# Kernel tuning notes

Hardware: AMD Instinct MI355X
Metric: run time of the kernel (lower is better)

The kernel has to match this reference:

```python
import jax, jax.numpy as jnp
import numpy as np

B, T, D = 16384, 7, 1024
H = D // 2          # LSTM hidden = 512
E = 64              # num_experts
TOPK = 8
NFLOW = 4


def setup_inputs() -> dict:
    key = jax.random.key(0)
    ks = jax.random.split(key, 16)
    s = 0.05
    return {
        'x': jax.random.normal(ks[0], (B, D), jnp.float32),
        'context': jax.random.normal(ks[1], (B, T, D), jnp.float32),
        # LSTM (PyTorch layout: [4H, in], gate order i,f,g,o)
        'W_ih': jax.random.normal(ks[2], (4 * H, D), jnp.float32) * s,
        'W_hh': jax.random.normal(ks[3], (4 * H, H), jnp.float32) * s,
        'b_ih': jnp.zeros((4 * H,), jnp.float32),
        'b_hh': jnp.zeros((4 * H,), jnp.float32),
        # flow_detector: Linear(D,H) -> ReLU -> Linear(H,4) -> softmax
        'fw1': jax.random.normal(ks[4], (H, D), jnp.float32) * s,
        'fb1': jnp.zeros((H,), jnp.float32),
        'fw2': jax.random.normal(ks[5], (NFLOW, H), jnp.float32) * s,
        'fb2': jnp.zeros((NFLOW,), jnp.float32),
        # main_gate: Linear(D+H+4, D) -> ReLU -> Linear(D, E)
        'gw1': jax.random.normal(ks[6], (D, D + H + NFLOW), jnp.float32) * s,
        'gb1': jnp.zeros((D,), jnp.float32),
        'gw2': jax.random.normal(ks[7], (E, D), jnp.float32) * s,
        'gb2': jnp.zeros((E,), jnp.float32),
        'expert_spec': jax.random.normal(ks[8], (E, NFLOW), jnp.float32) * 0.1,
    }


def _lstm_last_hidden(context, W_ih, W_hh, b_ih, b_hh):
    """Single-layer LSTM over [B,T,D]; returns last hidden state [B,H]."""
    b = b_ih + b_hh
    xs = jnp.einsum('btd,gd->tbg', context, W_ih) + b  # [T,B,4H], precompute input proj

    def step(carry, x_t):
        h, c = carry
        gates = x_t + h @ W_hh.T
        i, f, g, o = jnp.split(gates, 4, axis=-1)
        c = jax.nn.sigmoid(f) * c + jax.nn.sigmoid(i) * jnp.tanh(g)
        h = jax.nn.sigmoid(o) * jnp.tanh(c)
        return (h, c), None

    h0 = jnp.zeros((context.shape[0], H), context.dtype)
    (h, _), _ = jax.lax.scan(step, (h0, h0), xs)
    return h


def reference(x, context, W_ih, W_hh, b_ih, b_hh, fw1, fb1, fw2, fb2,
              gw1, gb1, gw2, gb2, expert_spec):
    context_feature = _lstm_last_hidden(context, W_ih, W_hh, b_ih, b_hh)  # [B,H]

    # flow_detector
    flow_state = jax.nn.softmax(
        jax.nn.relu(x @ fw1.T + fb1) @ fw2.T + fb2, axis=-1)  # [B,4]

    combined = jnp.concatenate([x, context_feature, flow_state], axis=-1)  # [B, D+H+4]
    gate_logits = jax.nn.relu(combined @ gw1.T + gb1) @ gw2.T + gb2  # [B,E]

    specialization = flow_state @ expert_spec.T  # [B,E]
    adjusted_logits = gate_logits + 0.1 * specialization
    gate_probs = jax.nn.softmax(adjusted_logits, axis=-1)

    top_k_probs, top_k_indices = jax.lax.top_k(gate_probs, TOPK)
    top_k_probs = top_k_probs / (top_k_probs.sum(-1, keepdims=True) + 1e-8)

    expert_usage = gate_probs.mean(0)  # [E]
    uniform = jnp.full_like(expert_usage, 1.0 / E)
    # F.kl_div(log_input, target, reduction='batchmean'): sum(t*(log t - log_input))/E
    load_balancing_loss = jnp.sum(
        uniform * (jnp.log(uniform) - jnp.log(expert_usage))) / E

    return (top_k_probs, top_k_indices, load_balancing_loss,
            flow_state, expert_usage, adjusted_logits)
```

## Files before the change

### kernel.cpp

```cpp
#include <hip/hip_runtime.h>
#include <cmath>

#define NB    16384
#define NT    7
#define ND    1024
#define NH    512
#define NE    64

#define OFF_WCAT   0ll
#define OFF_BLSTM  3145728ll
#define OFF_GW1P   3147776ll
#define OFF_FW1P   4737024ll
#define OFF_GW2T   5261312ll
#define OFF_H0     5326848ll
#define OFF_H1     13715456ll
#define OFF_C      22104064ll
#define OFF_HID    30492672ll
#define OFF_FLOW   47269888ll
#define OFF_UACC   47335424ll
#define WS_FLOATS  47335488ll

#define OUT_TOPKP  0ll
#define OUT_IDX    131072ll
#define OUT_LOSS   262144ll
#define OUT_FLOW   262145ll
#define OUT_USAGE  327681ll
#define OUT_ADJ    327745ll

__device__ __forceinline__ float sigm(float x) { return 1.0f / (1.0f + expf(-x)); }

__global__ void pack_lstm_k(const float* __restrict__ Wih, const float* __restrict__ Whh,
                            const float* __restrict__ bih, const float* __restrict__ bhh,
                            float* __restrict__ wcat, float* __restrict__ bl) {
  int idx = blockIdx.x * 256 + threadIdx.x;
  if (idx < 1536 * 2048) {
    int k = idx >> 11, n = idx & 2047;
    int u = n >> 2, g = n & 3;
    int r = g * 512 + u;
    wcat[idx] = (k < 1024) ? Wih[(size_t)r * 1024 + k] : Whh[(size_t)r * 512 + (k - 1024)];
  }
  if (idx < 2048) {
    int u = idx >> 2, g = idx & 3;
    int r = g * 512 + u;
    bl[idx] = bih[r] + bhh[r];
  }
}

__global__ void pack_gw1_k(const float* __restrict__ gw1, float* __restrict__ gw1p) {
  int idx = blockIdx.x * 256 + threadIdx.x;
  if (idx < 1552 * 1024) {
    int k = idx >> 10, n = idx & 1023;
    gw1p[idx] = (k < 1540) ? gw1[(size_t)n * 1540 + k] : 0.0f;
  }
}

__global__ void pack_fw1_k(const float* __restrict__ fw1, float* __restrict__ fw1p) {
  int idx = blockIdx.x * 256 + threadIdx.x;
  if (idx < 1024 * 512) {
    int k = idx >> 9, n = idx & 511;
    fw1p[idx] = fw1[(size_t)n * 1024 + k];
  }
}

__global__ void pack_gw2t_k(const float* __restrict__ gw2, float* __restrict__ gw2t) {
  int idx = blockIdx.x * 256 + threadIdx.x;
  if (idx < 1024 * 64) {
    int k = idx >> 6, e = idx & 63;
    gw2t[idx] = gw2[(size_t)e * 1024 + k];
  }
}

__device__ __forceinline__ float4 ldA4(const float* __restrict__ p0, int s0, int L0,
                                       const float* __restrict__ p1, int s1, int L01,
                                       const float* __restrict__ p2, int s2, int L012,
                                       int m, int k) {
  if (k < L0)   return *(const float4*)(p0 + (size_t)m * s0 + k);
  if (k < L01)  return *(const float4*)(p1 + (size_t)m * s1 + (k - L0));
  if (k < L012) return *(const float4*)(p2 + (size_t)m * s2 + (k - L01));
  return make_float4(0.f, 0.f, 0.f, 0.f);
}

template <int EPI>
__global__ __launch_bounds__(256) void gemm128(
    const float* __restrict__ p0, int s0, int L0,
    const float* __restrict__ p1, int s1, int L01,
    const float* __restrict__ p2, int s2, int L012,
    const float* __restrict__ Bp, int N, int nk,
    const float* __restrict__ bias,
    float* __restrict__ outp, int ldo,
    float* __restrict__ cbuf, float* __restrict__ hbuf, int first) {
  __shared__ __align__(16) float As[2][16][132];
  __shared__ __align__(16) float Bs[2][16][128];
  const int t = threadIdx.x;
  const int ntn = N >> 7;
  const int bn = blockIdx.x % ntn;
  const int bm = blockIdx.x / ntn;
  const int m0 = bm << 7, n0 = bn << 7;
  const int tx = t & 15, ty = t >> 4;
  const int lm = t & 127;
  const int kq = (t >> 7) << 3;
  const int lbk = t >> 5;
  const int lbn = (t & 31) << 2;
  const int am = m0 + lm;

  float acc[8][8];
#pragma unroll
  for (int i = 0; i < 8; i++)
#pragma unroll
    for (int j = 0; j < 8; j++) acc[i][j] = 0.f;

  float4 a0 = ldA4(p0, s0, L0, p1, s1, L01, p2, s2, L012, am, kq);
  float4 a1 = ldA4(p0, s0, L0, p1, s1, L01, p2, s2, L012, am, kq + 4);
  float4 b0 = *(const float4*)(Bp + (size_t)lbk * N + n0 + lbn);
  float4 b1 = *(const float4*)(Bp + (size_t)(lbk + 8) * N + n0 + lbn);

  As[0][kq + 0][lm] = a0.x; As[0][kq + 1][lm] = a0.y;
  As[0][kq + 2][lm] = a0.z; As[0][kq + 3][lm] = a0.w;
  As[0][kq + 4][lm] = a1.x; As[0][kq + 5][lm] = a1.y;
  As[0][kq + 6][lm] = a1.z; As[0][kq + 7][lm] = a1.w;
  *(float4*)&Bs[0][lbk][lbn] = b0;
  *(float4*)&Bs[0][lbk + 8][lbn] = b1;
  __syncthreads();

  int cur = 0;
  for (int kt = 0; kt < nk; ++kt) {
    const bool more = (kt + 1 < nk);
    if (more) {
      const int kb = (kt + 1) << 4;
      a0 = ldA4(p0, s0, L0, p1, s1, L01, p2, s2, L012, am, kb + kq);
      a1 = ldA4(p0, s0, L0, p1, s1, L01, p2, s2, L012, am, kb + kq + 4);
      b0 = *(const float4*)(Bp + (size_t)(kb + lbk) * N + n0 + lbn);
      b1 = *(const float4*)(Bp + (size_t)(kb + lbk + 8) * N + n0 + lbn);
    }
#pragma unroll
    for (int kk = 0; kk < 16; ++kk) {
      float4 av0 = *(const float4*)&As[cur][kk][ty << 3];
      float4 av1 = *(const float4*)&As[cur][kk][(ty << 3) + 4];
      float4 bv0 = *(const float4*)&Bs[cur][kk][tx << 3];
      float4 bv1 = *(const float4*)&Bs[cur][kk][(tx << 3) + 4];
      float ar[8] = {av0.x, av0.y, av0.z, av0.w, av1.x, av1.y, av1.z, av1.w};
      float br[8] = {bv0.x, bv0.y, bv0.z, bv0.w, bv1.x, bv1.y, bv1.z, bv1.w};
#pragma unroll
      for (int i = 0; i < 8; i++)
#pragma unroll
        for (int j = 0; j < 8; j++) acc[i][j] = fmaf(ar[i], br[j], acc[i][j]);
    }
    if (more) {
      const int nb2 = cur ^ 1;
      As[nb2][kq + 0][lm] = a0.x; As[nb2][kq + 1][lm] = a0.y;
      As[nb2][kq + 2][lm] = a0.z; As[nb2][kq + 3][lm] = a0.w;
      As[nb2][kq + 4][lm] = a1.x; As[nb2][kq + 5][lm] = a1.y;
      As[nb2][kq + 6][lm] = a1.z; As[nb2][kq + 7][lm] = a1.w;
      *(float4*)&Bs[nb2][lbk][lbn] = b0;
      *(float4*)&Bs[nb2][lbk + 8][lbn] = b1;
      __syncthreads();
      cur = nb2;
    }
  }

  float bv[8];
#pragma unroll
  for (int j = 0; j < 8; j++) bv[j] = bias[n0 + (tx << 3) + j];

  if (EPI == 0) {
#pragma unroll
    for (int i = 0; i < 8; i++) {
      const int m = m0 + (ty << 3) + i;
      float4 o0, o1;
      o0.x = fmaxf(acc[i][0] + bv[0], 0.f);
      o0.y = fmaxf(acc[i][1] + bv[1], 0.f);
      o0.z = fmaxf(acc[i][2] + bv[2], 0.f);
      o0.w = fmaxf(acc[i][3] + bv[3], 0.f);
      o1.x = fmaxf(acc[i][4] + bv[4], 0.f);
      o1.y = fmaxf(acc[i][5] + bv[5], 0.f);
      o1.z = fmaxf(acc[i][6] + bv[6], 0.f);
      o1.w = fmaxf(acc[i][7] + bv[7], 0.f);
      *(float4*)(outp + (size_t)m * ldo + n0 + (tx << 3)) = o0;
      *(float4*)(outp + (size_t)m * ldo + n0 + (tx << 3) + 4) = o1;
    }
  } else {
    const int u0 = (n0 + (tx << 3)) >> 2;
#pragma unroll
    for (int i = 0; i < 8; i++) {
      const int m = m0 + (ty << 3) + i;
#pragma unroll
      for (int p = 0; p < 2; p++) {
        const float ig = sigm(acc[i][4 * p + 0] + bv[4 * p + 0]);
        const float fg = sigm(acc[i][4 * p + 1] + bv[4 * p + 1]);
        const float gg = tanhf(acc[i][4 * p + 2] + bv[4 * p + 2]);
        const float og = sigm(acc[i][4 * p + 3] + bv[4 * p + 3]);
        const size_t off = (size_t)m * 512 + u0 + p;
        const float cold = first ? 0.f : cbuf[off];
        const float cn = fg * cold + ig * gg;
        cbuf[off] = cn;
        hbuf[off] = og * tanhf(cn);
      }
    }
  }
}

__global__ __launch_bounds__(256) void flow_head(
    const float* __restrict__ h1, const float* __restrict__ fw2,
    const float* __restrict__ fb2, float* __restrict__ fout,
    float* __restrict__ fws) {
  __shared__ float w[2048];
  const int t = threadIdx.x;
  for (int i = t; i < 2048; i += 256) w[i] = fw2[i];
  __syncthreads();
  const int wid = t >> 6, lane = t & 63;
  const int row = blockIdx.x * 4 + wid;
  const float* hr = h1 + (size_t)row * 512;
  float s0 = 0, s1 = 0, s2 = 0, s3 = 0;
#pragma unroll
  for (int j = 0; j < 8; j++) {
    const int k = j * 64 + lane;
    const float hv = hr[k];
    s0 = fmaf(hv, w[k], s0);
    s1 = fmaf(hv, w[512 + k], s1);
    s2 = fmaf(hv, w[1024 + k], s2);
    s3 = fmaf(hv, w[1536 + k], s3);
  }
  for (int off = 32; off; off >>= 1) {
    s0 += __shfl_xor(s0, off);
    s1 += __shfl_xor(s1, off);
    s2 += __shfl_xor(s2, off);
    s3 += __shfl_xor(s3, off);
  }
  const float l0 = s0 + fb2[0], l1 = s1 + fb2[1], l2 = s2 + fb2[2], l3 = s3 + fb2[3];
  const float mx = fmaxf(fmaxf(l0, l1), fmaxf(l2, l3));
  const float e0 = expf(l0 - mx), e1 = expf(l1 - mx), e2 = expf(l2 - mx), e3 = expf(l3 - mx);
  const float inv = 1.0f / (e0 + e1 + e2 + e3);
  if (lane < 4) {
    const float v = (lane == 0 ? e0 : lane == 1 ? e1 : lane == 2 ? e2 : e3) * inv;
    fout[(size_t)row * 4 + lane] = v;
    fws[(size_t)row * 4 + lane] = v;
  }
}

__global__ __launch_bounds__(256) void moe_head(
    const float* __restrict__ hid, const float* __restrict__ gw2t,
    const float* __restrict__ gb2, const float* __restrict__ spec,
    const float* __restrict__ flow, float* __restrict__ dout,
    float* __restrict__ uacc) {
  __shared__ __align__(16) float bs[8192];
  __shared__ float pbuf[256];
  const int t = threadIdx.x;
  const int wid = t >> 6, lane = t & 63;
  const int row = blockIdx.x * 4 + wid;
  const float* hr = hid + (size_t)row * 1024;
  float acc = 0.f;
  for (int kc = 0; kc < 8; ++kc) {
    __syncthreads();
    const float* src = gw2t + (size_t)kc * 8192;
#pragma unroll
    for (int q = 0; q < 8; q++) {
      const int o = q * 1024 + t * 4;
      *(float4*)&bs[o] = *(const float4*)&src[o];
    }
    __syncthreads();
    const float h0 = hr[kc * 128 + lane];
    const float h1v = hr[kc * 128 + 64 + lane];
#pragma unroll
    for (int kk = 0; kk < 64; kk++) acc = fmaf(__shfl(h0, kk), bs[kk * 64 + lane], acc);
#pragma unroll
    for (int kk = 0; kk < 64; kk++) acc = fmaf(__shfl(h1v, kk), bs[(64 + kk) * 64 + lane], acc);
  }
  const int e = lane;
  const float f0 = flow[(size_t)row * 4 + 0], f1 = flow[(size_t)row * 4 + 1];
  const float f2 = flow[(size_t)row * 4 + 2], f3 = flow[(size_t)row * 4 + 3];
  const float sp = f0 * spec[e * 4 + 0] + f1 * spec[e * 4 + 1] +
                   f2 * spec[e * 4 + 2] + f3 * spec[e * 4 + 3];
  const float adj = acc + gb2[e] + 0.1f * sp;
  dout[OUT_ADJ + (size_t)row * 64 + e] = adj;
  float mx = adj;
  for (int off = 32; off; off >>= 1) mx = fmaxf(mx, __shfl_xor(mx, off));
  const float pe = expf(adj - mx);
  float ssum = pe;
  for (int off = 32; off; off >>= 1) ssum += __shfl_xor(ssum, off);
  const float prob = pe / ssum;
  pbuf[wid * 64 + e] = prob;
  float v = prob;
  float selv = 0.f;
  int seli = 0;
  float s8 = 0.f;
#pragma unroll
  for (int it = 0; it < 8; ++it) {
    float bvv = v;
    int bi = e;
    for (int off = 32; off; off >>= 1) {
      const float ov = __shfl_xor(bvv, off);
      const int oi = __shfl_xor(bi, off);
      if (ov > bvv || (ov == bvv && oi < bi)) { bvv = ov; bi = oi; }
    }
    s8 += bvv;
    if (lane == it) { selv = bvv; seli = bi; }
    if (e == bi) v = -1.0f;
  }
  if (lane < 8) {
    dout[OUT_TOPKP + (size_t)row * 8 + lane] = selv / (s8 + 1e-8f);
    dout[OUT_IDX + (size_t)row * 8 + lane] = (float)seli;
  }
  __syncthreads();
  if (t < 64) {
    const float u = pbuf[t] + pbuf[64 + t] + pbuf[128 + t] + pbuf[192 + t];
    atomicAdd(&uacc[t], u);
  }
}

__global__ void finalize_k(const float* __restrict__ uacc, float* __restrict__ dout) {
  const int e = threadIdx.x;
  const float u = uacc[e] * (1.0f / 16384.0f);
  dout[OUT_USAGE + e] = u;
  float term = (logf(1.0f / 64.0f) - logf(u)) * (1.0f / 64.0f);
  for (int off = 32; off; off >>= 1) term += __shfl_xor(term, off);
  if (e == 0) dout[OUT_LOSS] = term * (1.0f / 64.0f);
}

extern "C" void kernel_launch(void* const* d_in, const int* in_sizes, int n_in,
                              void* d_out, int out_size, void* d_ws, size_t ws_size,
                              hipStream_t stream) {
  (void)in_sizes; (void)n_in; (void)out_size;
  if (ws_size < (size_t)WS_FLOATS * 4) return;

  const float* x    = (const float*)d_in[0];
  const float* ctx  = (const float*)d_in[1];
  const float* Wih  = (const float*)d_in[2];
  const float* Whh  = (const float*)d_in[3];
  const float* bih  = (const float*)d_in[4];
  const float* bhh  = (const float*)d_in[5];
  const float* fw1  = (const float*)d_in[6];
  const float* fb1  = (const float*)d_in[7];
  const float* fw2  = (const float*)d_in[8];
  const float* fb2  = (const float*)d_in[9];
  const float* gw1  = (const float*)d_in[10];
  const float* gb1  = (const float*)d_in[11];
  const float* gw2  = (const float*)d_in[12];
  const float* gb2  = (const float*)d_in[13];
  const float* spec = (const float*)d_in[14];
  float* out = (float*)d_out;
  float* ws = (float*)d_ws;

  float* wcat = ws + OFF_WCAT;
  float* bl   = ws + OFF_BLSTM;
  float* gw1p = ws + OFF_GW1P;
  float* fw1p = ws + OFF_FW1P;
  float* gw2t = ws + OFF_GW2T;
  float* H0   = ws + OFF_H0;
  float* H1   = ws + OFF_H1;
  float* C    = ws + OFF_C;
  float* HID  = ws + OFF_HID;
  float* FLW  = ws + OFF_FLOW;
  float* UA   = ws + OFF_UACC;

  hipMemsetAsync(UA, 0, 64 * sizeof(float), stream);
  pack_lstm_k<<<12288, 256, 0, stream>>>(Wih, Whh, bih, bhh, wcat, bl);
  pack_gw1_k<<<6208, 256, 0, stream>>>(gw1, gw1p);
  pack_fw1_k<<<2048, 256, 0, stream>>>(fw1, fw1p);
  pack_gw2t_k<<<256, 256, 0, stream>>>(gw2, gw2t);

  gemm128<0><<<128 * 4, 256, 0, stream>>>(x, 1024, 1024, x, 0, 1024, x, 0, 1024,
                                          fw1p, 512, 64, fb1, HID, 512,
                                          nullptr, nullptr, 0);
  flow_head<<<4096, 256, 0, stream>>>(HID, fw2, fb2, out + OUT_FLOW, FLW);

  for (int t = 0; t < 7; t++) {
    float* hout = (t & 1) ? H1 : H0;
    float* hin  = (t & 1) ? H0 : H1;
    const int K = t ? 1536 : 1024;
    gemm128<1><<<128 * 16, 256, 0, stream>>>(ctx + (size_t)t * 1024, 7168, 1024,
                                             hin, 512, K, hin, 0, K,
                                             wcat, 2048, K >> 4, bl, nullptr, 0,
                                             C, hout, t == 0 ? 1 : 0);
  }

  gemm128<0><<<128 * 8, 256, 0, stream>>>(x, 1024, 1024, H0, 512, 1536,
                                          FLW, 4, 1540, gw1p, 1024, 97, gb1,
                                          HID, 1024, nullptr, nullptr, 0);

  moe_head<<<4096, 256, 0, stream>>>(HID, gw2t, gb2, spec, FLW, out, UA);
  finalize_k<<<1, 64, 0, stream>>>(UA, out);
}
```

Before: 14.24 ms.

## Load B tiles directly into LDS and remap thread column ownership

B-operand tiles in the FP32 SGEMM are now fetched with global_load_lds, which writes straight into shared memory instead of passing through registers and separate LDS stores. Each thread's columns are remapped from 8 contiguous columns to two 4-wide groups 64 apart, which is meant to reduce LDS bank conflicts on B reads. The bias and LSTM-epilogue indexing are updated to match. The async load must be complete before the __syncthreads, and there is no explicit vmcnt wait, which risks a data race.

```diff
diff --git a/kernel.cpp b/kernel.cpp
--- a/kernel.cpp
+++ b/kernel.cpp
@@ -28,6 +28,11 @@
 #define OUT_ADJ    327745ll
 
 __device__ __forceinline__ float sigm(float x) { return 1.0f / (1.0f + expf(-x)); }
+
+__device__ __forceinline__ void gload_lds16(const float* __restrict__ g, float* s) {
+  __builtin_amdgcn_global_load_lds((const __attribute__((address_space(1))) void*)g,
+                                   (__attribute__((address_space(3))) void*)s, 16, 0, 0);
+}
 
 __global__ void pack_lstm_k(const float* __restrict__ Wih, const float* __restrict__ Whh,
                             const float* __restrict__ bih, const float* __restrict__ bhh,
@@ -109,17 +114,14 @@
 #pragma unroll
     for (int j = 0; j < 8; j++) acc[i][j] = 0.f;
 
+  gload_lds16(Bp + (size_t)lbk * N + n0 + lbn, &Bs[0][lbk][lbn]);
+  gload_lds16(Bp + (size_t)(lbk + 8) * N + n0 + lbn, &Bs[0][lbk + 8][lbn]);
   float4 a0 = ldA4(p0, s0, L0, p1, s1, L01, p2, s2, L012, am, kq);
   float4 a1 = ldA4(p0, s0, L0, p1, s1, L01, p2, s2, L012, am, kq + 4);
-  float4 b0 = *(const float4*)(Bp + (size_t)lbk * N + n0 + lbn);
-  float4 b1 = *(const float4*)(Bp + (size_t)(lbk + 8) * N + n0 + lbn);
-
   As[0][kq + 0][lm] = a0.x; As[0][kq + 1][lm] = a0.y;
   As[0][kq + 2][lm] = a0.z; As[0][kq + 3][lm] = a0.w;
   As[0][kq + 4][lm] = a1.x; As[0][kq + 5][lm] = a1.y;
   As[0][kq + 6][lm] = a1.z; As[0][kq + 7][lm] = a1.w;
-  *(float4*)&Bs[0][lbk][lbn] = b0;
-  *(float4*)&Bs[0][lbk + 8][lbn] = b1;
   __syncthreads();
 
   int cur = 0;
@@ -127,17 +129,17 @@
     const bool more = (kt + 1 < nk);
     if (more) {
       const int kb = (kt + 1) << 4;
+      gload_lds16(Bp + (size_t)(kb + lbk) * N + n0 + lbn, &Bs[cur ^ 1][lbk][lbn]);
+      gload_lds16(Bp + (size_t)(kb + lbk + 8) * N + n0 + lbn, &Bs[cur ^ 1][lbk + 8][lbn]);
       a0 = ldA4(p0, s0, L0, p1, s1, L01, p2, s2, L012, am, kb + kq);
       a1 = ldA4(p0, s0, L0, p1, s1, L01, p2, s2, L012, am, kb + kq + 4);
-      b0 = *(const float4*)(Bp + (size_t)(kb + lbk) * N + n0 + lbn);
-      b1 = *(const float4*)(Bp + (size_t)(kb + lbk + 8) * N + n0 + lbn);
     }
 #pragma unroll
     for (int kk = 0; kk < 16; ++kk) {
       float4 av0 = *(const float4*)&As[cur][kk][ty << 3];
       float4 av1 = *(const float4*)&As[cur][kk][(ty << 3) + 4];
-      float4 bv0 = *(const float4*)&Bs[cur][kk][tx << 3];
-      float4 bv1 = *(const float4*)&Bs[cur][kk][(tx << 3) + 4];
+      float4 bv0 = *(const float4*)&Bs[cur][kk][tx << 2];
+      float4 bv1 = *(const float4*)&Bs[cur][kk][64 + (tx << 2)];
       float ar[8] = {av0.x, av0.y, av0.z, av0.w, av1.x, av1.y, av1.z, av1.w};
       float br[8] = {bv0.x, bv0.y, bv0.z, bv0.w, bv1.x, bv1.y, bv1.z, bv1.w};
 #pragma unroll
@@ -151,45 +153,45 @@
       As[nb2][kq + 2][lm] = a0.z; As[nb2][kq + 3][lm] = a0.w;
       As[nb2][kq + 4][lm] = a1.x; As[nb2][kq + 5][lm] = a1.y;
       As[nb2][kq + 6][lm] = a1.z; As[nb2][kq + 7][lm] = a1.w;
-      *(float4*)&Bs[nb2][lbk][lbn] = b0;
-      *(float4*)&Bs[nb2][lbk + 8][lbn] = b1;
       __syncthreads();
       cur = nb2;
     }
   }
 
-  float bv[8];
-#pragma unroll
-  for (int j = 0; j < 8; j++) bv[j] = bias[n0 + (tx << 3) + j];
+  const int c0 = n0 + (tx << 2);
+  float ba[4], bb[4];
+#pragma unroll
+  for (int j = 0; j < 4; j++) { ba[j] = bias[c0 + j]; bb[j] = bias[c0 + 64 + j]; }
 
   if (EPI == 0) {
 #pragma unroll
     for (int i = 0; i < 8; i++) {
       const int m = m0 + (ty << 3) + i;
       float4 o0, o1;
-      o0.x = fmaxf(acc[i][0] + bv[0], 0.f);
-      o0.y = fmaxf(acc[i][1] + bv[1], 0.f);
-      o0.z = fmaxf(acc[i][2] + bv[2], 0.f);
-      o0.w = fmaxf(acc[i][3] + bv[3], 0.f);
-      o1.x = fmaxf(acc[i][4] + bv[4], 0.f);
-      o1.y = fmaxf(acc[i][5] + bv[5], 0.f);
-      o1.z = fmaxf(acc[i][6] + bv[6], 0.f);
-      o1.w = fmaxf(acc[i][7] + bv[7], 0.f);
-      *(float4*)(outp + (size_t)m * ldo + n0 + (tx << 3)) = o0;
-      *(float4*)(outp + (size_t)m * ldo + n0 + (tx << 3) + 4) = o1;
+      o0.x = fmaxf(acc[i][0] + ba[0], 0.f);
+      o0.y = fmaxf(acc[i][1] + ba[1], 0.f);
+      o0.z = fmaxf(acc[i][2] + ba[2], 0.f);
+      o0.w = fmaxf(acc[i][3] + ba[3], 0.f);
+      o1.x = fmaxf(acc[i][4] + bb[0], 0.f);
+      o1.y = fmaxf(acc[i][5] + bb[1], 0.f);
+      o1.z = fmaxf(acc[i][6] + bb[2], 0.f);
+      o1.w = fmaxf(acc[i][7] + bb[3], 0.f);
+      *(float4*)(outp + (size_t)m * ldo + c0) = o0;
+      *(float4*)(outp + (size_t)m * ldo + c0 + 64) = o1;
     }
   } else {
-    const int u0 = (n0 + (tx << 3)) >> 2;
+    const int ub = (n0 >> 2) + tx;
 #pragma unroll
     for (int i = 0; i < 8; i++) {
       const int m = m0 + (ty << 3) + i;
 #pragma unroll
       for (int p = 0; p < 2; p++) {
-        const float ig = sigm(acc[i][4 * p + 0] + bv[4 * p + 0]);
-        const float fg = sigm(acc[i][4 * p + 1] + bv[4 * p + 1]);
-        const float gg = tanhf(acc[i][4 * p + 2] + bv[4 * p + 2]);
-        const float og = sigm(acc[i][4 * p + 3] + bv[4 * p + 3]);
-        const size_t off = (size_t)m * 512 + u0 + p;
+        const float* bq = p ? bb : ba;
+        const float ig = sigm(acc[i][4 * p + 0] + bq[0]);
+        const float fg = sigm(acc[i][4 * p + 1] + bq[1]);
+        const float gg = tanhf(acc[i][4 * p + 2] + bq[2]);
+        const float og = sigm(acc[i][4 * p + 3] + bq[3]);
+        const size_t off = (size_t)m * 512 + ub + 16 * p;
         const float cold = first ? 0.f : cbuf[off];
         const float cn = fg * cold + ig * gg;
         cbuf[off] = cn;
```

After: 13.93 ms. 1.02x faster.
